# Optimization experiments

Hardware: AMD Instinct MI355X
Metric: run time of the kernel (lower is better)

## Reference

```python
import jax, jax.numpy as jnp
import numpy as np

N_EMBD = 1024
N_HEAD = 16
HEAD_SIZE = N_EMBD // N_HEAD  # 64
B, T = 4, 2048

def setup_inputs() -> dict:
    key = jax.random.key(0)
    k1, k2, k3, k4 = jax.random.split(key, 4)
    x = jax.random.normal(k1, (B, T, N_EMBD), dtype=jnp.float32)
    # weights stored as [in, out]; torch Linear does x @ W.T with W [out,in]
    w_qkv = jax.random.normal(k2, (N_EMBD, 3 * N_EMBD), dtype=jnp.float32) * (N_EMBD ** -0.5)
    w_proj = jax.random.normal(k3, (N_EMBD, N_EMBD), dtype=jnp.float32) * (N_EMBD ** -0.5)
    b_proj = jax.random.normal(k4, (N_EMBD,), dtype=jnp.float32) * 0.01
    return {"x": x, "w_qkv": w_qkv, "w_proj": w_proj, "b_proj": b_proj}

def reference(x, w_qkv, w_proj, b_proj):
    Bx, Tx, C = x.shape
    H, D = N_HEAD, HEAD_SIZE
    qkv = x @ w_qkv                               # [B,T,3C]
    q, k, v = jnp.split(qkv, 3, axis=-1)
    q = q.reshape(Bx, Tx, H, D).transpose(0, 2, 1, 3)  # [B,H,T,D]
    k = k.reshape(Bx, Tx, H, D).transpose(0, 2, 1, 3)
    v = v.reshape(Bx, Tx, H, D).transpose(0, 2, 1, 3)
    att = jnp.einsum('bhqd,bhkd->bhqk', q, k) * (D ** -0.5)  # [B,H,T,T]
    causal = jnp.tril(jnp.ones((Tx, Tx), dtype=bool))
    att = jnp.where(causal[None, None], att, -jnp.inf)
    att = jax.nn.softmax(att, axis=-1)
    out = jnp.einsum('bhqk,bhkd->bhqd', att, v)   # [B,H,T,D]
    out = out.transpose(0, 2, 1, 3).reshape(Bx, Tx, H * D)
    return out @ w_proj + b_proj
```

## Files before the change

### kernel.cpp

```cpp
#include <hip/hip_runtime.h>
#include <hip/hip_bf16.h>
#include <stdint.h>
#include <math.h>


typedef __attribute__((ext_vector_type(8))) short short8;
typedef __attribute__((ext_vector_type(4))) float f32x4;

#define LOG2E 1.44269504088896340736f
#define QSCALE 0.18033688011112042f

__device__ int g_isf32;

__device__ __forceinline__ void gl16(const void* g, void* l) {
  __builtin_amdgcn_global_load_lds(
      (const __attribute__((address_space(1))) unsigned int*)g,
      (__attribute__((address_space(3))) unsigned int*)l, 16, 0, 0);
}

__device__ __forceinline__ short f2bf(float f) {
  __hip_bfloat16 h = __float2bfloat16(f);
  return *reinterpret_cast<short*>(&h);
}
__device__ __forceinline__ float bf2f(short s) {
  __hip_bfloat16 h = *reinterpret_cast<__hip_bfloat16*>(&s);
  return __bfloat162float(h);
}
__device__ __forceinline__ short8 pack8(f32x4 lo, f32x4 hi) {
  short8 r;
#pragma unroll
  for (int e = 0; e < 4; ++e) { r[e] = f2bf(lo[e]); r[4 + e] = f2bf(hi[e]); }
  return r;
}

__device__ __forceinline__ short pbf(float f) {
  unsigned u = __builtin_bit_cast(unsigned, f);
  return (short)((u + 0x8000u) >> 16);
}

__device__ __forceinline__ float dpp_max16(float x) {
  int i;
  i = __builtin_amdgcn_update_dpp(0, __builtin_bit_cast(int, x), 0xB1, 0xF, 0xF, true);
  x = fmaxf(x, __builtin_bit_cast(float, i));
  i = __builtin_amdgcn_update_dpp(0, __builtin_bit_cast(int, x), 0x4E, 0xF, 0xF, true);
  x = fmaxf(x, __builtin_bit_cast(float, i));
  i = __builtin_amdgcn_update_dpp(0, __builtin_bit_cast(int, x), 0x141, 0xF, 0xF, true);
  x = fmaxf(x, __builtin_bit_cast(float, i));
  i = __builtin_amdgcn_update_dpp(0, __builtin_bit_cast(int, x), 0x140, 0xF, 0xF, true);
  x = fmaxf(x, __builtin_bit_cast(float, i));
  return x;
}
__device__ __forceinline__ float dpp_sum16(float x) {
  int i;
  i = __builtin_amdgcn_update_dpp(0, __builtin_bit_cast(int, x), 0xB1, 0xF, 0xF, true);
  x += __builtin_bit_cast(float, i);
  i = __builtin_amdgcn_update_dpp(0, __builtin_bit_cast(int, x), 0x4E, 0xF, 0xF, true);
  x += __builtin_bit_cast(float, i);
  i = __builtin_amdgcn_update_dpp(0, __builtin_bit_cast(int, x), 0x141, 0xF, 0xF, true);
  x += __builtin_bit_cast(float, i);
  i = __builtin_amdgcn_update_dpp(0, __builtin_bit_cast(int, x), 0x140, 0xF, 0xF, true);
  x += __builtin_bit_cast(float, i);
  return x;
}

__global__ __launch_bounds__(256) void detect_dtype(const unsigned short* w) {
  __shared__ int cnt;
  if (threadIdx.x == 0) cnt = 0;
  __syncthreads();
  const unsigned short* p = w + (long)blockIdx.x * 49152;
  int c = 0;
  for (int i = threadIdx.x; i < 49152; i += 256)
    if (((p[i] >> 7) & 0xFF) == 0xFF) c++;
  atomicAdd(&cnt, c);
  __syncthreads();
  if (threadIdx.x == 0) g_isf32 = (cnt > 8) ? 1 : 0;
}

__global__ __launch_bounds__(256) void cvt_x(const void* __restrict__ src,
                                             short* __restrict__ dst) {
  const long i = ((long)blockIdx.x * 256 + threadIdx.x) * 8;
  if (g_isf32) {
    const float* s = (const float*)src + i;
    *(short8*)(dst + i) = pack8(*(const f32x4*)s, *(const f32x4*)(s + 4));
  } else {
    *(short8*)(dst + i) = *(const short8*)((const short*)src + i);
  }
}

template <int MODE>
__global__ __launch_bounds__(256) void gemm_bt(
    const short* __restrict__ A, const short* __restrict__ Bt,
    const void* __restrict__ bias, void* __restrict__ C,
    short* __restrict__ vt, int M, int N, int K)
{
  __shared__ __align__(16) short As[128 * 32];
  __shared__ __align__(16) short Bs[128 * 32];
  const int isf32 = g_isf32;
  const int tid  = threadIdx.x;
  const int lane = tid & 63;
  const int wave = tid >> 6;
  const int quad = lane >> 4;
  const int l16  = lane & 15;
  const int wm = (wave & 1) * 64;
  const int wn = (wave >> 1) * 64;
  const long m0 = (long)blockIdx.y * 128;
  const long n0 = (long)blockIdx.x * 128;

  f32x4 acc[4][4] = {};

  const int r4 = tid >> 2;
  const int c4 = tid & 3;
  const short* Ag = A  + (m0 + r4) * (long)K + c4 * 8;
  const short* Bg = Bt + (n0 + r4) * (long)K + c4 * 8;
  const long rowskip = (long)64 * K;

  for (int k0 = 0; k0 < K; k0 += 32) {
    __syncthreads();
    gl16(Ag + k0,           (char*)As + tid * 16);
    gl16(Ag + k0 + rowskip, (char*)As + 4096 + tid * 16);
    gl16(Bg + k0,           (char*)Bs + tid * 16);
    gl16(Bg + k0 + rowskip, (char*)Bs + 4096 + tid * 16);
    __syncthreads();
    short8 af[4], bfv[4];
#pragma unroll
    for (int i = 0; i < 4; ++i)
      af[i] = *(const short8*)&As[(wm + i * 16 + l16) * 32 + quad * 8];
#pragma unroll
    for (int j = 0; j < 4; ++j)
      bfv[j] = *(const short8*)&Bs[(wn + j * 16 + l16) * 32 + quad * 8];
#pragma unroll
    for (int i = 0; i < 4; ++i)
#pragma unroll
      for (int j = 0; j < 4; ++j)
        acc[i][j] = __builtin_amdgcn_mfma_f32_16x16x32_bf16(af[i], bfv[j], acc[i][j], 0, 0, 0);
  }

#pragma unroll
  for (int j = 0; j < 4; ++j) {
    const long col = n0 + wn + j * 16 + l16;
    float bv = 0.f;
    if (MODE == 1)
      bv = isf32 ? ((const float*)bias)[col] : bf2f(((const short*)bias)[col]);
#pragma unroll
    for (int i = 0; i < 4; ++i) {
      const long row0 = m0 + wm + i * 16 + quad * 4;
#pragma unroll
      for (int r = 0; r < 4; ++r) {
        const long row = row0 + r;
        const float val = acc[i][j][r] + bv;
        if (MODE == 2) {
          if (col < 2048) {
            const float vq = (col < 1024) ? val * QSCALE : val;
            ((short*)C)[row * 2048 + col] = f2bf(vq);
          } else {
            const long b = row >> 11, t = row & 2047;
            const long hd = col - 2048;
            vt[((b * 16 + (hd >> 6)) * 64 + (hd & 63)) * 2048 + t] = f2bf(val);
          }
        } else {
          if (isf32) ((float*)C)[row * (long)N + col] = val;
          else       ((short*)C)[row * (long)N + col] = f2bf(val);
        }
      }
    }
  }
}

__global__ __launch_bounds__(256) void transpose64(
    const void* __restrict__ src, short* __restrict__ dst, int R, int C)
{
  __shared__ __align__(16) short tile[64][72];
  const int isf32 = g_isf32;
  const int tid = threadIdx.x;
  const long r0 = (long)blockIdx.y * 64;
  const long c0 = (long)blockIdx.x * 64;
#pragma unroll
  for (int it = 0; it < 2; ++it) {
    int idx = it * 256 + tid;
    int rr = idx >> 3, ch = idx & 7;
    const long off = (r0 + rr) * C + c0 + ch * 8;
    short8 v;
    if (isf32) {
      const float* s = (const float*)src + off;
      v = pack8(*(const f32x4*)s, *(const f32x4*)(s + 4));
    } else {
      v = *(const short8*)((const short*)src + off);
    }
    *(short8*)&tile[rr][ch * 8] = v;
  }
  __syncthreads();
#pragma unroll
  for (int it = 0; it < 2; ++it) {
    int idx = it * 256 + tid;
    int cc = idx >> 3, ch = idx & 7;
    short8 v;
#pragma unroll
    for (int jj = 0; jj < 8; ++jj) v[jj] = tile[ch * 8 + jj][cc];
    *(short8*)&dst[(c0 + cc) * R + r0 + ch * 8] = v;
  }
}

__global__ __launch_bounds__(256) void attn_fwd(
    const short* __restrict__ qk, const short* __restrict__ vt,
    short* __restrict__ out)
{
  __shared__ __align__(16) short Ks[2][64][32];
  __shared__ __align__(16) short Vs[2][64][32];
  __shared__ __align__(16) short Pw[4][16][76];
  const int tid = threadIdx.x;
  const int lane = tid & 63, wave = tid >> 6;
  const int quad = lane >> 4, l16 = lane & 15;
  const int bh = blockIdx.x;
  const int b = bh >> 4, h = bh & 15;
  const int jq = (int)gridDim.y - 1 - (int)blockIdx.y;
  const int qbase = jq * 64 + wave * 16;

  const short* qp = qk + ((long)(b * 2048 + qbase + l16)) * 2048 + h * 64 + quad * 8;
  const short8 aq0 = *(const short8*)qp;
  const short8 aq1 = *(const short8*)(qp + 32);

  const int sr = tid >> 2, sc_ = tid & 3;
  const short* kg = qk + (long)b * 2048 * 2048 + 1024 + h * 64 + (long)sr * 2048 + sc_ * 8;
  const short* vg = vt + ((long)bh * 64 + sr) * 2048 + sc_ * 8;

  f32x4 o[4] = {};
  float m_run[4], l_run[4];
#pragma unroll
  for (int r = 0; r < 4; ++r) { m_run[r] = -1e30f; l_run[r] = 0.f; }

  for (int kt = 0; kt < jq; ++kt) {
    const int k0 = kt * 64;

    __syncthreads();
    gl16(kg + (long)k0 * 2048,      (char*)Ks + tid * 16);
    gl16(kg + (long)k0 * 2048 + 32, (char*)Ks + 4096 + tid * 16);
    gl16(vg + k0,                   (char*)Vs + tid * 16);
    gl16(vg + k0 + 32,              (char*)Vs + 4096 + tid * 16);
    __syncthreads();

    f32x4 s[4];
#pragma unroll
    for (int c = 0; c < 4; ++c) {
      short8 kf0 = *(const short8*)&Ks[0][c * 16 + l16][quad * 8];
      short8 kf1 = *(const short8*)&Ks[1][c * 16 + l16][quad * 8];
      f32x4 z = {};
      z = __builtin_amdgcn_mfma_f32_16x16x32_bf16(aq0, kf0, z, 0, 0, 0);
      z = __builtin_amdgcn_mfma_f32_16x16x32_bf16(aq1, kf1, z, 0, 0, 0);
      s[c] = z;
    }

    float mx[4];
#pragma unroll
    for (int r = 0; r < 4; ++r)
      mx[r] = dpp_max16(fmaxf(fmaxf(s[0][r], s[1][r]), fmaxf(s[2][r], s[3][r])));

    int grow = 0;
#pragma unroll
    for (int r = 0; r < 4; ++r) grow |= (mx[r] > m_run[r] + 8.f);
    if (__any(grow)) {
#pragma unroll
      for (int r = 0; r < 4; ++r) {
        const float mn = fmaxf(m_run[r], mx[r]);
        const float al = __builtin_amdgcn_exp2f(m_run[r] - mn);
        m_run[r] = mn;
        l_run[r] *= al;
#pragma unroll
        for (int i = 0; i < 4; ++i) o[i][r] *= al;
      }
    }

#pragma unroll
    for (int c = 0; c < 4; ++c)
#pragma unroll
      for (int r = 0; r < 4; ++r) {
        const float p = __builtin_amdgcn_exp2f(s[c][r] - m_run[r]);
        l_run[r] += p;
        Pw[wave][quad * 4 + r][c * 16 + l16] = pbf(p);
      }

    {
      short8 pf0 = *(const short8*)&Pw[wave][l16][quad * 8];
      short8 pf1 = *(const short8*)&Pw[wave][l16][32 + quad * 8];
#pragma unroll
      for (int i = 0; i < 4; ++i) {
        short8 vf0 = *(const short8*)&Vs[0][i * 16 + l16][quad * 8];
        o[i] = __builtin_amdgcn_mfma_f32_16x16x32_bf16(pf0, vf0, o[i], 0, 0, 0);
        short8 vf1 = *(const short8*)&Vs[1][i * 16 + l16][quad * 8];
        o[i] = __builtin_amdgcn_mfma_f32_16x16x32_bf16(pf1, vf1, o[i], 0, 0, 0);
      }
    }
  }

  {
    const int k0 = jq * 64;

    __syncthreads();
    gl16(kg + (long)k0 * 2048,      (char*)Ks + tid * 16);
    gl16(kg + (long)k0 * 2048 + 32, (char*)Ks + 4096 + tid * 16);
    gl16(vg + k0,                   (char*)Vs + tid * 16);
    gl16(vg + k0 + 32,              (char*)Vs + 4096 + tid * 16);
    __syncthreads();

    f32x4 s[4];
    float mx[4];
#pragma unroll
    for (int r = 0; r < 4; ++r) mx[r] = -1e30f;
#pragma unroll
    for (int c = 0; c < 4; ++c) {
      if (c > wave) continue;
      short8 kf0 = *(const short8*)&Ks[0][c * 16 + l16][quad * 8];
      short8 kf1 = *(const short8*)&Ks[1][c * 16 + l16][quad * 8];
      f32x4 z = {};
      z = __builtin_amdgcn_mfma_f32_16x16x32_bf16(aq0, kf0, z, 0, 0, 0);
      z = __builtin_amdgcn_mfma_f32_16x16x32_bf16(aq1, kf1, z, 0, 0, 0);
      if (c == wave) {
#pragma unroll
        for (int r = 0; r < 4; ++r)
          z[r] = (l16 > quad * 4 + r) ? -1e30f : z[r];
      }
      s[c] = z;
#pragma unroll
      for (int r = 0; r < 4; ++r) mx[r] = fmaxf(mx[r], z[r]);
    }
#pragma unroll
    for (int r = 0; r < 4; ++r) mx[r] = dpp_max16(mx[r]);

    int grow = 0;
#pragma unroll
    for (int r = 0; r < 4; ++r) grow |= (mx[r] > m_run[r] + 8.f);
    if (__any(grow)) {
#pragma unroll
      for (int r = 0; r < 4; ++r) {
        const float mn = fmaxf(m_run[r], mx[r]);
        const float al = __builtin_amdgcn_exp2f(m_run[r] - mn);
        m_run[r] = mn;
        l_run[r] *= al;
#pragma unroll
        for (int i = 0; i < 4; ++i) o[i][r] *= al;
      }
    }

#pragma unroll
    for (int c = 0; c < 4; ++c) {
      if (c <= wave) {
#pragma unroll
        for (int r = 0; r < 4; ++r) {
          const float p = __builtin_amdgcn_exp2f(s[c][r] - m_run[r]);
          l_run[r] += p;
          Pw[wave][quad * 4 + r][c * 16 + l16] = pbf(p);
        }
      } else if (c < 2 || wave >= 2) {
#pragma unroll
        for (int r = 0; r < 4; ++r)
          Pw[wave][quad * 4 + r][c * 16 + l16] = 0;
      }
    }

    {
      short8 pf0 = *(const short8*)&Pw[wave][l16][quad * 8];
#pragma unroll
      for (int i = 0; i < 4; ++i) {
        short8 vf0 = *(const short8*)&Vs[0][i * 16 + l16][quad * 8];
        o[i] = __builtin_amdgcn_mfma_f32_16x16x32_bf16(pf0, vf0, o[i], 0, 0, 0);
      }
      if (wave >= 2) {
        short8 pf1 = *(const short8*)&Pw[wave][l16][32 + quad * 8];
#pragma unroll
        for (int i = 0; i < 4; ++i) {
          short8 vf1 = *(const short8*)&Vs[1][i * 16 + l16][quad * 8];
          o[i] = __builtin_amdgcn_mfma_f32_16x16x32_bf16(pf1, vf1, o[i], 0, 0, 0);
        }
      }
    }
  }

#pragma unroll
  for (int r = 0; r < 4; ++r) l_run[r] = dpp_sum16(l_run[r]);
  float inv[4];
#pragma unroll
  for (int r = 0; r < 4; ++r) inv[r] = 1.0f / l_run[r];
  short* op = out + ((long)(b * 2048 + qbase + quad * 4)) * 1024 + h * 64;
#pragma unroll
  for (int i = 0; i < 4; ++i)
#pragma unroll
    for (int r = 0; r < 4; ++r)
      op[(long)r * 1024 + i * 16 + l16] = f2bf(o[i][r] * inv[r]);
}

__global__ __launch_bounds__(256) void copy_out(const void* __restrict__ src,
                                                void* __restrict__ dst)
{
  const long n16 = g_isf32 ? 2097152L : 1048576L;
  const uint4* s = (const uint4*)src;
  uint4* d = (uint4*)dst;
  for (long i = (long)blockIdx.x * 256 + threadIdx.x; i < n16;
       i += (long)gridDim.x * 256)
    d[i] = s[i];
}

extern "C" void kernel_launch(void* const* d_in, const int* in_sizes, int n_in,
                              void* d_out, int out_size, void* d_ws, size_t ws_size,
                              hipStream_t stream)
{
  const void* x      = d_in[0];
  const void* w_qkv  = d_in[1];
  const void* w_proj = d_in[2];
  const void* b_proj = d_in[3];

  short* ws = (short*)d_ws;
  const bool planA = ws_size >= 67108864ULL;

  short* qk  = ws;
  short* vtp = ws + 16777216L;

  short *wqkvT, *attnb, *wprojT, *xbf;
  void*  projC;
  if (planA) {
    attnb  = ws + 25165824L;
    wqkvT  = attnb;
    wprojT = qk;
    xbf    = (short*)d_out;
    projC  = d_out;
  } else {
    wqkvT  = (short*)d_out;
    xbf    = (short*)d_out + 3145728L;
    attnb  = (short*)d_out;
    wprojT = vtp;
    projC  = qk;
  }

  detect_dtype<<<64, 256, 0, stream>>>((const unsigned short*)w_qkv);
  cvt_x<<<4096, 256, 0, stream>>>(x, xbf);
  transpose64<<<dim3(3072 / 64, 1024 / 64), 256, 0, stream>>>(w_qkv, wqkvT, 1024, 3072);
  gemm_bt<2><<<dim3(3072 / 128, 8192 / 128), 256, 0, stream>>>(
      xbf, wqkvT, nullptr, qk, vtp, 8192, 3072, 1024);
  attn_fwd<<<dim3(64, 32), 256, 0, stream>>>(qk, vtp, attnb);
  transpose64<<<dim3(1024 / 64, 1024 / 64), 256, 0, stream>>>(w_proj, wprojT, 1024, 1024);
  gemm_bt<1><<<dim3(1024 / 128, 8192 / 128), 256, 0, stream>>>(
      attnb, wprojT, b_proj, projC, nullptr, 8192, 1024, 1024);
  if (!planA)
    copy_out<<<2048, 256, 0, stream>>>(projC, d_out);
}
```

Baseline: 330.4 us.

## Double-buffer GEMM LDS tiles with XOR swizzle, K=64 steps and XCD remap

```diff
diff --git a/kernel.cpp b/kernel.cpp
--- a/kernel.cpp
+++ b/kernel.cpp
@@ -88,13 +88,13 @@
 }
 
 template <int MODE>
-__global__ __launch_bounds__(256) void gemm_bt(
+__global__ __launch_bounds__(256, 2) void gemm_bt(
     const short* __restrict__ A, const short* __restrict__ Bt,
     const void* __restrict__ bias, void* __restrict__ C,
     short* __restrict__ vt, int M, int N, int K)
 {
-  __shared__ __align__(16) short As[128 * 32];
-  __shared__ __align__(16) short Bs[128 * 32];
+  __shared__ __align__(16) short As[2][8192];
+  __shared__ __align__(16) short Bs[2][8192];
   const int isf32 = g_isf32;
   const int tid  = threadIdx.x;
   const int lane = tid & 63;
@@ -103,36 +103,77 @@
   const int l16  = lane & 15;
   const int wm = (wave & 1) * 64;
   const int wn = (wave >> 1) * 64;
-  const long m0 = (long)blockIdx.y * 128;
-  const long n0 = (long)blockIdx.x * 128;
+
+  const int gx = (int)gridDim.x;
+  const int nwg = gx * (int)gridDim.y;
+  int lb = (int)blockIdx.y * gx + (int)blockIdx.x;
+  if ((nwg & 7) == 0) lb = (lb & 7) * (nwg >> 3) + (lb >> 3);
+  const long m0 = (long)(lb / gx) * 128;
+  const long n0 = (long)(lb % gx) * 128;
 
   f32x4 acc[4][4] = {};
 
-  const int r4 = tid >> 2;
-  const int c4 = tid & 3;
-  const short* Ag = A  + (m0 + r4) * (long)K + c4 * 8;
-  const short* Bg = Bt + (n0 + r4) * (long)K + c4 * 8;
-  const long rowskip = (long)64 * K;
-
-  for (int k0 = 0; k0 < K; k0 += 32) {
+  const int r0 = tid >> 3;
+  const int c0 = (tid & 7) ^ (r0 & 7);
+  const short* Ag = A  + (m0 + r0) * (long)K + c0 * 8;
+  const short* Bg = Bt + (n0 + r0) * (long)K + c0 * 8;
+  const long rs = (long)32 * K;
+
+  const int x7  = l16 & 7;
+  const int xo0 = ((quad)     ^ x7) * 16;
+  const int xo1 = ((4 + quad) ^ x7) * 16;
+  const int aRowB = (wm + l16) * 128;
+  const int bRowB = (wn + l16) * 128;
+
+#pragma unroll
+  for (int g = 0; g < 4; ++g) {
+    gl16(Ag + g * rs, (char*)As + g * 4096 + tid * 16);
+    gl16(Bg + g * rs, (char*)Bs + g * 4096 + tid * 16);
+  }
+  __syncthreads();
+
+  const int nt = K >> 6;
+  for (int t = 0; t < nt; ++t) {
+    const int p = t & 1;
+    if (t + 1 < nt) {
+      const long k1 = (long)(t + 1) << 6;
+      char* Ad = (char*)As + (p ^ 1) * 16384;
+      char* Bd = (char*)Bs + (p ^ 1) * 16384;
+#pragma unroll
+      for (int g = 0; g < 4; ++g) {
+        gl16(Ag + k1 + g * rs, Ad + g * 4096 + tid * 16);
+        gl16(Bg + k1 + g * rs, Bd + g * 4096 + tid * 16);
+      }
+    }
+    const char* Ab = (const char*)As + p * 16384;
+    const char* Bb = (const char*)Bs + p * 16384;
+    short8 bf[4][2];
+#pragma unroll
+    for (int j = 0; j < 4; ++j) {
+      bf[j][0] = *(const short8*)(Bb + bRowB + j * 2048 + xo0);
+      bf[j][1] = *(const short8*)(Bb + bRowB + j * 2048 + xo1);
+    }
+#pragma unroll
+    for (int ph = 0; ph < 2; ++ph) {
+      short8 af[2][2];
+#pragma unroll
+      for (int dm = 0; dm < 2; ++dm) {
+        const int i = ph * 2 + dm;
+        af[dm][0] = *(const short8*)(Ab + aRowB + i * 2048 + xo0);
+        af[dm][1] = *(const short8*)(Ab + aRowB + i * 2048 + xo1);
+      }
+      __builtin_amdgcn_s_setprio(1);
+#pragma unroll
+      for (int dm = 0; dm < 2; ++dm)
+#pragma unroll
+        for (int j = 0; j < 4; ++j) {
+          const int i = ph * 2 + dm;
+          acc[i][j] = __builtin_amdgcn_mfma_f32_16x16x32_bf16(af[dm][0], bf[j][0], acc[i][j], 0, 0, 0);
+          acc[i][j] = __builtin_amdgcn_mfma_f32_16x16x32_bf16(af[dm][1], bf[j][1], acc[i][j], 0, 0, 0);
+        }
+      __builtin_amdgcn_s_setprio(0);
+    }
     __syncthreads();
-    gl16(Ag + k0,           (char*)As + tid * 16);
-    gl16(Ag + k0 + rowskip, (char*)As + 4096 + tid * 16);
-    gl16(Bg + k0,           (char*)Bs + tid * 16);
-    gl16(Bg + k0 + rowskip, (char*)Bs + 4096 + tid * 16);
-    __syncthreads();
-    short8 af[4], bfv[4];
-#pragma unroll
-    for (int i = 0; i < 4; ++i)
-      af[i] = *(const short8*)&As[(wm + i * 16 + l16) * 32 + quad * 8];
-#pragma unroll
-    for (int j = 0; j < 4; ++j)
-      bfv[j] = *(const short8*)&Bs[(wn + j * 16 + l16) * 32 + quad * 8];
-#pragma unroll
-    for (int i = 0; i < 4; ++i)
-#pragma unroll
-      for (int j = 0; j < 4; ++j)
-        acc[i][j] = __builtin_amdgcn_mfma_f32_16x16x32_bf16(af[i], bfv[j], acc[i][j], 0, 0, 0);
   }
 
 #pragma unroll
```

Measured after the change: 310.6 us. -6.0%, faster.

## Restructure GEMM with 256x128 tiles, triple-buffered async LDS loads, XOR swizzle

Applied to the files above, without the earlier changes.

```diff
diff --git a/kernel.cpp b/kernel.cpp
--- a/kernel.cpp
+++ b/kernel.cpp
@@ -88,51 +88,92 @@
 }
 
 template <int MODE>
-__global__ __launch_bounds__(256) void gemm_bt(
+__global__ __launch_bounds__(512, 2) void gemm_bt(
     const short* __restrict__ A, const short* __restrict__ Bt,
     const void* __restrict__ bias, void* __restrict__ C,
     short* __restrict__ vt, int M, int N, int K)
 {
-  __shared__ __align__(16) short As[128 * 32];
-  __shared__ __align__(16) short Bs[128 * 32];
-  const int isf32 = g_isf32;
+  __shared__ __align__(16) short As[3][16384];
+  __shared__ __align__(16) short Bs[3][8192];
   const int tid  = threadIdx.x;
   const int lane = tid & 63;
   const int wave = tid >> 6;
   const int quad = lane >> 4;
   const int l16  = lane & 15;
-  const int wm = (wave & 1) * 64;
-  const int wn = (wave >> 1) * 64;
-  const long m0 = (long)blockIdx.y * 128;
-  const long n0 = (long)blockIdx.x * 128;
+  const int wm = (wave >> 1) * 64;
+  const int wn = (wave & 1) * 64;
+
+  const int gx = (int)gridDim.x;
+  const int nwg = gx * (int)gridDim.y;
+  int lb = (int)blockIdx.y * gx + (int)blockIdx.x;
+  if ((nwg & 7) == 0) lb = (lb & 7) * (nwg >> 3) + (lb >> 3);
+  const long m0 = (long)(lb / gx) * 256;
+  const long n0 = (long)(lb % gx) * 128;
+
+  int isf32 = 0;
+  if (MODE == 1) {
+    isf32 = g_isf32;
+    asm volatile("s_waitcnt vmcnt(0) lgkmcnt(0)" ::: "memory");
+  }
 
   f32x4 acc[4][4] = {};
 
-  const int r4 = tid >> 2;
-  const int c4 = tid & 3;
-  const short* Ag = A  + (m0 + r4) * (long)K + c4 * 8;
-  const short* Bg = Bt + (n0 + r4) * (long)K + c4 * 8;
-  const long rowskip = (long)64 * K;
-
-  for (int k0 = 0; k0 < K; k0 += 32) {
-    __syncthreads();
-    gl16(Ag + k0,           (char*)As + tid * 16);
-    gl16(Ag + k0 + rowskip, (char*)As + 4096 + tid * 16);
-    gl16(Bg + k0,           (char*)Bs + tid * 16);
-    gl16(Bg + k0 + rowskip, (char*)Bs + 4096 + tid * 16);
-    __syncthreads();
-    short8 af[4], bfv[4];
+  const int srow = tid >> 3;
+  const int scol = ((tid & 7) ^ (srow & 7)) * 8;
+  const short* Ag = A  + (m0 + srow) * (long)K + scol;
+  const short* Bg = Bt + (n0 + srow) * (long)K + scol;
+  const long rs64 = (long)64 * K;
+
+  const int x7  = l16 & 7;
+  const int xo0 = ((0 + quad) ^ x7) * 16;
+  const int xo1 = ((4 + quad) ^ x7) * 16;
+  const int aRow = (wm + l16) * 128;
+  const int bRow = (wn + l16) * 128;
+
+  auto STAGE = [&](int t) {
+    const int b = t % 3;
+    const long k0 = (long)t << 6;
+#pragma unroll
+    for (int g = 0; g < 4; ++g)
+      gl16(Ag + k0 + g * rs64, (char*)As[b] + g * 8192 + tid * 16);
+#pragma unroll
+    for (int g = 0; g < 2; ++g)
+      gl16(Bg + k0 + g * rs64, (char*)Bs[b] + g * 8192 + tid * 16);
+  };
+
+  const int nt = K >> 6;
+  STAGE(0);
+  STAGE(1);
+
+  for (int t = 0; t < nt; ++t) {
+    if (t + 1 < nt) { asm volatile("s_waitcnt vmcnt(6)" ::: "memory"); }
+    else            { asm volatile("s_waitcnt vmcnt(0)" ::: "memory"); }
+    __builtin_amdgcn_sched_barrier(0);
+    __builtin_amdgcn_s_barrier();
+    if (t + 2 < nt) STAGE(t + 2);
+
+    const char* Ab = (const char*)As[t % 3];
+    const char* Bb = (const char*)Bs[t % 3];
+    short8 af[4][2], bfv[4][2];
+#pragma unroll
+    for (int i = 0; i < 4; ++i) {
+      af[i][0] = *(const short8*)(Ab + aRow + i * 2048 + xo0);
+      af[i][1] = *(const short8*)(Ab + aRow + i * 2048 + xo1);
+    }
+#pragma unroll
+    for (int j = 0; j < 4; ++j) {
+      bfv[j][0] = *(const short8*)(Bb + bRow + j * 2048 + xo0);
+      bfv[j][1] = *(const short8*)(Bb + bRow + j * 2048 + xo1);
+    }
+    __builtin_amdgcn_s_setprio(1);
 #pragma unroll
     for (int i = 0; i < 4; ++i)
-      af[i] = *(const short8*)&As[(wm + i * 16 + l16) * 32 + quad * 8];
-#pragma unroll
-    for (int j = 0; j < 4; ++j)
-      bfv[j] = *(const short8*)&Bs[(wn + j * 16 + l16) * 32 + quad * 8];
-#pragma unroll
-    for (int i = 0; i < 4; ++i)
-#pragma unroll
-      for (int j = 0; j < 4; ++j)
-        acc[i][j] = __builtin_amdgcn_mfma_f32_16x16x32_bf16(af[i], bfv[j], acc[i][j], 0, 0, 0);
+#pragma unroll
+      for (int j = 0; j < 4; ++j) {
+        acc[i][j] = __builtin_amdgcn_mfma_f32_16x16x32_bf16(af[i][0], bfv[j][0], acc[i][j], 0, 0, 0);
+        acc[i][j] = __builtin_amdgcn_mfma_f32_16x16x32_bf16(af[i][1], bfv[j][1], acc[i][j], 0, 0, 0);
+      }
+    __builtin_amdgcn_s_setprio(0);
   }
 
 #pragma unroll
@@ -432,11 +473,11 @@
   detect_dtype<<<64, 256, 0, stream>>>((const unsigned short*)w_qkv);
   cvt_x<<<4096, 256, 0, stream>>>(x, xbf);
   transpose64<<<dim3(3072 / 64, 1024 / 64), 256, 0, stream>>>(w_qkv, wqkvT, 1024, 3072);
-  gemm_bt<2><<<dim3(3072 / 128, 8192 / 128), 256, 0, stream>>>(
+  gemm_bt<2><<<dim3(3072 / 128, 8192 / 256), 512, 0, stream>>>(
       xbf, wqkvT, nullptr, qk, vtp, 8192, 3072, 1024);
   attn_fwd<<<dim3(64, 32), 256, 0, stream>>>(qk, vtp, attnb);
   transpose64<<<dim3(1024 / 64, 1024 / 64), 256, 0, stream>>>(w_proj, wprojT, 1024, 1024);
-  gemm_bt<1><<<dim3(1024 / 128, 8192 / 128), 256, 0, stream>>>(
+  gemm_bt<1><<<dim3(1024 / 128, 8192 / 256), 512, 0, stream>>>(
       attnb, wprojT, b_proj, projC, nullptr, 8192, 1024, 1024);
   if (!planA)
     copy_out<<<2048, 256, 0, stream>>>(projC, d_out);
```

New measurement: 321.2 us. 2.8% less time.
